# Optimization experiments

Measured on AMD Instinct MI355X. Metric: run time of the kernel, lower is better.

## Reference

```python
import jax, jax.numpy as jnp
import numpy as np


def hadamard(D):
    # Sylvester Hadamard: H[i,j] = (-1)^popcount(i & j), normalized by sqrt(D)
    x = np.arange(D)[:, None] & np.arange(D)[None, :]
    par = np.zeros_like(x)
    for _ in range(int(np.log2(D)) + 1):
        par ^= x & 1
        x >>= 1
    return ((1.0 - 2.0 * par) / np.sqrt(D)).astype(np.float32)


def setup_inputs() -> dict:
    key = jax.random.key(0)
    ks = jax.random.split(key, 6)
    K, M, D, T = 4, 32, 2048, 128
    z = jax.random.normal(ks[0], (K, M, D, T), dtype=jnp.float32)
    d1 = jax.random.normal(ks[1], (D, 1), dtype=jnp.float32)
    d2 = jax.random.normal(ks[2], (D, 1), dtype=jnp.float32)
    d3 = jax.random.normal(ks[3], (D, 1), dtype=jnp.float32)
    b = jax.random.normal(ks[4], (D, 1), dtype=jnp.float32)
    sldj = jax.random.normal(ks[5], (K * M,), dtype=jnp.float32)
    return {"z": z, "d1": d1, "d2": d2, "d3": d3, "b": b,
            "sum_log_det_jacobians": sldj}


def reference(z, d1, d2, d3, b, sum_log_det_jacobians):
    K, M, D, T = z.shape
    H = jnp.asarray(hadamard(D), dtype=z.dtype)
    # A = H @ D3 @ H @ D2 @ H @ D1
    #   H @ diag(d)  == H * d.T (scale columns)
    #   diag(d) @ X  == d * X   (scale rows)
    A = H @ (d3 * (H @ (d2 * (H * d1[:, 0][None, :]))))
    # apply: tensordot(A, z, [[1],[2]]) then transpose to (K,M,D,T), add bias
    z_out = jnp.einsum('de,kmet->kmdt', A, z) + b[None, None, :, :]
    # log|det A| = sum_i log|d1_i| + log|d2_i| + log|d3_i|  (H is orthogonal)
    log_det_A = (jnp.sum(jnp.log(jnp.abs(d1)))
                 + jnp.sum(jnp.log(jnp.abs(d2)))
                 + jnp.sum(jnp.log(jnp.abs(d3))))
    sldj = sum_log_det_jacobians + log_det_A * jnp.ones((K * M,), dtype=z.dtype)
    return z_out, sldj
```

## Files before the change

### kernel.cpp

```cpp
#include <hip/hip_runtime.h>
#include <math.h>

#define D_DIM 2048
#define T_DIM 128
#define TT 8

__device__ __forceinline__ int esw(int e) {
    return e ^ ((((e >> 2) ^ (e >> 5)) & 1) | (((e >> 6) & 1) << 1));
}

#define BFLY(MM)                                              \
    _Pragma("unroll")                                         \
    for (int i_ = 0; i_ < 64; ++i_) {                         \
        if ((i_ & (MM)) == 0) {                               \
            float a_ = v[i_], b_ = v[i_ | (MM)];              \
            v[i_] = a_ + b_;                                  \
            v[i_ | (MM)] = a_ - b_;                           \
        }                                                     \
    }

__global__ __launch_bounds__(256, 2)
void fwht_apply_kernel(const float* __restrict__ z,
                       const float* __restrict__ d1,
                       const float* __restrict__ d2,
                       const float* __restrict__ d3,
                       const float* __restrict__ bvec,
                       float* __restrict__ out) {
    __shared__ float lds[D_DIM * TT];
    const int tid = threadIdx.x;
    const int r   = tid >> 3;
    const int tt  = tid & 7;
    const int bid = blockIdx.x;
    const int km  = bid >> 4;
    const int t0  = (bid & 15) << 3;
    const float s = 0.022097086912079608f;

    const float* zb = z + ((size_t)km * D_DIM) * T_DIM + t0 + tt;
    float v[64];

    #pragma unroll
    for (int j = 0; j < 64; ++j) {
        const int e = (j << 5) | r;
        v[j] = zb[(size_t)e * T_DIM] * (d1[e] * s);
    }
    BFLY(1) BFLY(2) BFLY(4) BFLY(8) BFLY(16) BFLY(32)

    #pragma unroll
    for (int j = 0; j < 64; ++j) {
        const int e = (j << 5) | r;
        lds[esw(e) * TT + tt] = v[j];
    }
    __syncthreads();

    #pragma unroll
    for (int j = 0; j < 64; ++j) {
        const int e = (j & 31) | ((j >> 5) << 10) | (r << 5);
        v[j] = lds[esw(e) * TT + tt];
    }
    __syncthreads();
    BFLY(1) BFLY(2) BFLY(4) BFLY(8) BFLY(16)
    {
        const float4* q0 = (const float4*)(d2 + (r << 5));
        const float4* q1 = (const float4*)(d2 + 1024 + (r << 5));
        #pragma unroll
        for (int q = 0; q < 8; ++q) {
            float4 a = q0[q];
            v[4*q+0] *= a.x * s; v[4*q+1] *= a.y * s;
            v[4*q+2] *= a.z * s; v[4*q+3] *= a.w * s;
            float4 c = q1[q];
            v[32+4*q+0] *= c.x * s; v[32+4*q+1] *= c.y * s;
            v[32+4*q+2] *= c.z * s; v[32+4*q+3] *= c.w * s;
        }
    }
    BFLY(1) BFLY(2) BFLY(4) BFLY(8) BFLY(16) BFLY(32)

    #pragma unroll
    for (int j = 0; j < 64; ++j) {
        const int e = (j & 31) | ((j >> 5) << 10) | (r << 5);
        lds[esw(e) * TT + tt] = v[j];
    }
    __syncthreads();

    const int eRest = ((r & 15) << 1) | ((r >> 4) << 10);
    #pragma unroll
    for (int j = 0; j < 64; ++j) {
        const int e = ((j & 31) << 5) | (j >> 5) | eRest;
        v[j] = lds[esw(e) * TT + tt];
    }
    __syncthreads();
    BFLY(1) BFLY(2) BFLY(4) BFLY(8) BFLY(16)
    {
        #pragma unroll
        for (int j = 0; j < 32; ++j) {
            float2 a = *(const float2*)(d3 + ((j << 5) | eRest));
            v[j]      *= a.x * s;
            v[j + 32] *= a.y * s;
        }
    }
    BFLY(1) BFLY(2) BFLY(4) BFLY(8) BFLY(16) BFLY(32)

    #pragma unroll
    for (int j = 0; j < 64; ++j) {
        const int e = ((j & 31) << 5) | (j >> 5) | eRest;
        lds[esw(e) * TT + tt] = v[j];
    }
    __syncthreads();

    #pragma unroll
    for (int j = 0; j < 64; ++j) {
        const int e = (j & 31) | ((j >> 5) << 10) | (r << 5);
        v[j] = lds[esw(e) * TT + tt];
    }
    BFLY(2) BFLY(4) BFLY(8) BFLY(16) BFLY(32)

    float* ob = out + ((size_t)km * D_DIM) * T_DIM + t0 + tt;
    {
        const float4* q0 = (const float4*)(bvec + (r << 5));
        const float4* q1 = (const float4*)(bvec + 1024 + (r << 5));
        #pragma unroll
        for (int q = 0; q < 8; ++q) {
            float4 a = q0[q];
            const int e0 = (r << 5) + 4*q;
            ob[(size_t)(e0+0) * T_DIM] = v[4*q+0] + a.x;
            ob[(size_t)(e0+1) * T_DIM] = v[4*q+1] + a.y;
            ob[(size_t)(e0+2) * T_DIM] = v[4*q+2] + a.z;
            ob[(size_t)(e0+3) * T_DIM] = v[4*q+3] + a.w;
            float4 c = q1[q];
            const int e1 = 1024 + (r << 5) + 4*q;
            ob[(size_t)(e1+0) * T_DIM] = v[32+4*q+0] + c.x;
            ob[(size_t)(e1+1) * T_DIM] = v[32+4*q+1] + c.y;
            ob[(size_t)(e1+2) * T_DIM] = v[32+4*q+2] + c.z;
            ob[(size_t)(e1+3) * T_DIM] = v[32+4*q+3] + c.w;
        }
    }
}

__global__ void sldj_kernel(const float* __restrict__ d1,
                            const float* __restrict__ d2,
                            const float* __restrict__ d3,
                            const float* __restrict__ sldj_in,
                            float* __restrict__ out) {
    __shared__ float red[256];
    const int tid = threadIdx.x;
    float acc = 0.0f;
    for (int i = tid; i < D_DIM; i += 256) {
        acc += logf(fabsf(d1[i])) + logf(fabsf(d2[i])) + logf(fabsf(d3[i]));
    }
    red[tid] = acc;
    __syncthreads();
    #pragma unroll
    for (int sft = 128; sft > 0; sft >>= 1) {
        if (tid < sft) red[tid] += red[tid + sft];
        __syncthreads();
    }
    const float tot = red[0];
    if (tid < 128) out[tid] = sldj_in[tid] + tot;
}

extern "C" void kernel_launch(void* const* d_in, const int* in_sizes, int n_in,
                              void* d_out, int out_size, void* d_ws, size_t ws_size,
                              hipStream_t stream) {
    const float* z    = (const float*)d_in[0];
    const float* d1   = (const float*)d_in[1];
    const float* d2   = (const float*)d_in[2];
    const float* d3   = (const float*)d_in[3];
    const float* bvec = (const float*)d_in[4];
    const float* sldj = (const float*)d_in[5];
    float* out = (float*)d_out;

    fwht_apply_kernel<<<2048, 256, 0, stream>>>(z, d1, d2, d3, bvec, out);
    sldj_kernel<<<1, 256, 0, stream>>>(d1, d2, d3, sldj,
                                       out + (size_t)4 * 32 * 2048 * 128);
}
```

Measured before the change: 323.2 us.

## Widen FWHT tile to 16 columns and split LDS transposes into half-sized passes

Each block now covers 16 time columns with 512 threads instead of 8 columns with 256 threads, so global loads and stores are 64 bytes contiguous per row instead of 32. To keep LDS usage at 64KB, each transpose is split into two half passes over a 1024-row buffer, with simpler XOR swizzles and reordered butterfly stages. The aim is better coalescing and occupancy. The cost is twice as many barriers and a register-heavy 64-value array at 512 threads per block, which risks spills under launch_bounds(512,4).

```diff
diff --git a/kernel.cpp b/kernel.cpp
--- a/kernel.cpp
+++ b/kernel.cpp
@@ -3,11 +3,10 @@
 
 #define D_DIM 2048
 #define T_DIM 128
-#define TT 8
+#define TT 16
 
-__device__ __forceinline__ int esw(int e) {
-    return e ^ ((((e >> 2) ^ (e >> 5)) & 1) | (((e >> 6) & 1) << 1));
-}
+__device__ __forceinline__ int sw1(int x) { return x ^ ((x >> 5) & 1); }
+__device__ __forceinline__ int sw2(int x) { return x ^ ((x >> 4) & 1); }
 
 #define BFLY(MM)                                              \
     _Pragma("unroll")                                         \
@@ -19,20 +18,20 @@
         }                                                     \
     }
 
-__global__ __launch_bounds__(256, 2)
+__global__ __launch_bounds__(512, 4)
 void fwht_apply_kernel(const float* __restrict__ z,
                        const float* __restrict__ d1,
                        const float* __restrict__ d2,
                        const float* __restrict__ d3,
                        const float* __restrict__ bvec,
                        float* __restrict__ out) {
-    __shared__ float lds[D_DIM * TT];
+    __shared__ float lds[1024 * TT];
     const int tid = threadIdx.x;
-    const int r   = tid >> 3;
-    const int tt  = tid & 7;
+    const int r   = tid >> 4;
+    const int tt  = tid & 15;
     const int bid = blockIdx.x;
-    const int km  = bid >> 4;
-    const int t0  = (bid & 15) << 3;
+    const int km  = bid >> 3;
+    const int t0  = (bid & 7) << 4;
     const float s = 0.022097086912079608f;
 
     const float* zb = z + ((size_t)km * D_DIM) * T_DIM + t0 + tt;
@@ -46,18 +45,22 @@
     BFLY(1) BFLY(2) BFLY(4) BFLY(8) BFLY(16) BFLY(32)
 
     #pragma unroll
-    for (int j = 0; j < 64; ++j) {
-        const int e = (j << 5) | r;
-        lds[esw(e) * TT + tt] = v[j];
-    }
+    for (int j = 0; j < 32; ++j)
+        lds[sw1((j << 5) | r) * TT + tt] = v[j];
+    __syncthreads();
+    #pragma unroll
+    for (int j = 0; j < 32; ++j)
+        v[j] = lds[sw1(j | (r << 5)) * TT + tt];
+    __syncthreads();
+    #pragma unroll
+    for (int j = 32; j < 64; ++j)
+        lds[sw1(((j & 31) << 5) | r) * TT + tt] = v[j];
+    __syncthreads();
+    #pragma unroll
+    for (int j = 32; j < 64; ++j)
+        v[j] = lds[sw1((j & 31) | (r << 5)) * TT + tt];
     __syncthreads();
 
-    #pragma unroll
-    for (int j = 0; j < 64; ++j) {
-        const int e = (j & 31) | ((j >> 5) << 10) | (r << 5);
-        v[j] = lds[esw(e) * TT + tt];
-    }
-    __syncthreads();
     BFLY(1) BFLY(2) BFLY(4) BFLY(8) BFLY(16)
     {
         const float4* q0 = (const float4*)(d2 + (r << 5));
@@ -75,42 +78,50 @@
     BFLY(1) BFLY(2) BFLY(4) BFLY(8) BFLY(16) BFLY(32)
 
     #pragma unroll
-    for (int j = 0; j < 64; ++j) {
-        const int e = (j & 31) | ((j >> 5) << 10) | (r << 5);
-        lds[esw(e) * TT + tt] = v[j];
-    }
+    for (int j = 0; j < 64; j += 2)
+        lds[sw2(((j >> 1) & 15) | (r << 4) | ((j >> 5) << 9)) * TT + tt] = v[j];
+    __syncthreads();
+    #pragma unroll
+    for (int j = 0; j < 64; j += 2)
+        v[j] = lds[sw2((((j >> 1) & 31) << 4) | (r & 15) | ((r >> 4) << 9)) * TT + tt];
+    __syncthreads();
+    #pragma unroll
+    for (int j = 1; j < 64; j += 2)
+        lds[sw2(((j >> 1) & 15) | (r << 4) | ((j >> 5) << 9)) * TT + tt] = v[j];
+    __syncthreads();
+    #pragma unroll
+    for (int j = 1; j < 64; j += 2)
+        v[j] = lds[sw2((((j >> 1) & 31) << 4) | (r & 15) | ((r >> 4) << 9)) * TT + tt];
     __syncthreads();
 
-    const int eRest = ((r & 15) << 1) | ((r >> 4) << 10);
-    #pragma unroll
-    for (int j = 0; j < 64; ++j) {
-        const int e = ((j & 31) << 5) | (j >> 5) | eRest;
-        v[j] = lds[esw(e) * TT + tt];
-    }
-    __syncthreads();
-    BFLY(1) BFLY(2) BFLY(4) BFLY(8) BFLY(16)
+    BFLY(2) BFLY(4) BFLY(8) BFLY(16) BFLY(32)
     {
+        const int eRest = ((r & 15) << 1) | ((r >> 4) << 10);
         #pragma unroll
-        for (int j = 0; j < 32; ++j) {
-            float2 a = *(const float2*)(d3 + ((j << 5) | eRest));
-            v[j]      *= a.x * s;
-            v[j + 32] *= a.y * s;
+        for (int m = 0; m < 32; ++m) {
+            float2 a = *(const float2*)(d3 + ((m << 5) | eRest));
+            v[2*m]   *= a.x * s;
+            v[2*m+1] *= a.y * s;
         }
     }
-    BFLY(1) BFLY(2) BFLY(4) BFLY(8) BFLY(16) BFLY(32)
+    BFLY(2) BFLY(4) BFLY(8) BFLY(16) BFLY(32) BFLY(1)
 
     #pragma unroll
-    for (int j = 0; j < 64; ++j) {
-        const int e = ((j & 31) << 5) | (j >> 5) | eRest;
-        lds[esw(e) * TT + tt] = v[j];
-    }
+    for (int j = 0; j < 64; j += 2)
+        lds[sw2((((j >> 1) & 31) << 4) | (r & 15) | ((r >> 4) << 9)) * TT + tt] = v[j];
     __syncthreads();
+    #pragma unroll
+    for (int j = 0; j < 64; j += 2)
+        v[j] = lds[sw2(((j >> 1) & 15) | (r << 4) | ((j >> 5) << 9)) * TT + tt];
+    __syncthreads();
+    #pragma unroll
+    for (int j = 1; j < 64; j += 2)
+        lds[sw2((((j >> 1) & 31) << 4) | (r & 15) | ((r >> 4) << 9)) * TT + tt] = v[j];
+    __syncthreads();
+    #pragma unroll
+    for (int j = 1; j < 64; j += 2)
+        v[j] = lds[sw2(((j >> 1) & 15) | (r << 4) | ((j >> 5) << 9)) * TT + tt];
 
-    #pragma unroll
-    for (int j = 0; j < 64; ++j) {
-        const int e = (j & 31) | ((j >> 5) << 10) | (r << 5);
-        v[j] = lds[esw(e) * TT + tt];
-    }
     BFLY(2) BFLY(4) BFLY(8) BFLY(16) BFLY(32)
 
     float* ob = out + ((size_t)km * D_DIM) * T_DIM + t0 + tt;
@@ -168,7 +179,7 @@
     const float* sldj = (const float*)d_in[5];
     float* out = (float*)d_out;
 
-    fwht_apply_kernel<<<2048, 256, 0, stream>>>(z, d1, d2, d3, bvec, out);
+    fwht_apply_kernel<<<1024, 512, 0, stream>>>(z, d1, d2, d3, bvec, out);
     sldj_kernel<<<1, 256, 0, stream>>>(d1, d2, d3, sldj,
                                        out + (size_t)4 * 32 * 2048 * 128);
 }
```

Result: no change. 327.9 us (+1.4%).
